# Optimization experiments

Hardware: AMD Instinct MI355X
Metric: run time of the kernel (lower is better)

## Reference

```python
import jax, jax.numpy as jnp
import numpy as np

D = 128        # node_state_dim
F = 10         # len(CHOSEN_CONNECTION_FEATURES)
N_IP = 20000
N_CONN = 100000
E = 200000
T = 3


def _seg_mean(vals, ids, n):
    s = jax.ops.segment_sum(vals, ids, num_segments=n)
    c = jax.ops.segment_sum(jnp.ones((vals.shape[0], 1), vals.dtype), ids, num_segments=n)
    return s / jnp.maximum(c, 1.0)


def _gru(x, h, kernel, rec_kernel, bias):
    # keras GRUCell, reset_after=True, gate order [z, r, hh]
    xm = x @ kernel + bias[0]
    hm = h @ rec_kernel + bias[1]
    xz, xr, xh = jnp.split(xm, 3, axis=-1)
    hz, hr, hh = jnp.split(hm, 3, axis=-1)
    z = jax.nn.sigmoid(xz + hz)
    r = jax.nn.sigmoid(xr + hr)
    hcand = jnp.tanh(xh + r * hh)
    return z * h + (1.0 - z) * hcand


def setup_inputs() -> dict:
    key = jax.random.key(0)
    ks = jax.random.split(key, 24)
    s = 0.02
    inp = {
        "feature_connection": jax.random.normal(ks[0], (N_CONN, F), jnp.float32),
        "src_ip_to_connection": jax.random.randint(ks[1], (E,), 0, N_IP, jnp.int32),
        "dst_ip_to_connection": jax.random.randint(ks[2], (E,), 0, N_CONN, jnp.int32),
        "src_connection_to_ip": jax.random.randint(ks[3], (E,), 0, N_CONN, jnp.int32),
        "dst_connection_to_ip": jax.random.randint(ks[4], (E,), 0, N_IP, jnp.int32),
        # message MLPs
        "W_m1": jax.random.normal(ks[5], (2 * D, D), jnp.float32) * s,
        "b_m1": jnp.zeros((D,), jnp.float32),
        "W_m2": jax.random.normal(ks[6], (2 * D, D), jnp.float32) * s,
        "b_m2": jnp.zeros((D,), jnp.float32),
        # GRU cells
        "gru_ip_k": jax.random.normal(ks[7], (D, 3 * D), jnp.float32) * s,
        "gru_ip_r": jax.random.normal(ks[8], (D, 3 * D), jnp.float32) * s,
        "gru_ip_b": jnp.zeros((2, 3 * D), jnp.float32),
        "gru_c_k": jax.random.normal(ks[9], (D, 3 * D), jnp.float32) * s,
        "gru_c_r": jax.random.normal(ks[10], (D, 3 * D), jnp.float32) * s,
        "gru_c_b": jnp.zeros((2, 3 * D), jnp.float32),
        # readout MLP
        "W_r1": jax.random.normal(ks[11], (D, 128), jnp.float32) * s,
        "b_r1": jnp.zeros((128,), jnp.float32),
        "W_r2": jax.random.normal(ks[12], (128, 64), jnp.float32) * s,
        "b_r2": jnp.zeros((64,), jnp.float32),
        "W_r3": jax.random.normal(ks[13], (64, 15), jnp.float32) * s,
        "b_r3": jnp.zeros((15,), jnp.float32),
    }
    return inp


def reference(feature_connection, src_ip_to_connection, dst_ip_to_connection,
              src_connection_to_ip, dst_connection_to_ip,
              W_m1, b_m1, W_m2, b_m2,
              gru_ip_k, gru_ip_r, gru_ip_b,
              gru_c_k, gru_c_r, gru_c_b,
              W_r1, b_r1, W_r2, b_r2, W_r3, b_r3):
    ip_state = jnp.ones((N_IP, D), jnp.float32)
    connection_state = jnp.concatenate(
        [feature_connection, jnp.zeros((N_CONN, D - F), jnp.float32)], axis=1)

    for _ in range(T):
        # ip -> connection messages
        nn_in = jnp.concatenate([ip_state[src_ip_to_connection],
                                 connection_state[dst_ip_to_connection]], axis=1)
        ip_message = jax.nn.relu(nn_in @ W_m1 + b_m1)            # [E, D]
        ip_mean = _seg_mean(ip_message, dst_ip_to_connection, N_CONN)
        # connection -> ip messages
        nn_in2 = jnp.concatenate([connection_state[src_connection_to_ip],
                                  ip_state[dst_connection_to_ip]], axis=1)
        conn_message = jax.nn.relu(nn_in2 @ W_m2 + b_m2)         # [E, D]
        conn_mean = _seg_mean(conn_message, dst_connection_to_ip, N_IP)
        # GRU updates
        ip_state = _gru(conn_mean, ip_state, gru_ip_k, gru_ip_r, gru_ip_b)
        connection_state = _gru(ip_mean, connection_state, gru_c_k, gru_c_r, gru_c_b)

    h = jax.nn.relu(connection_state @ W_r1 + b_r1)
    h = jax.nn.relu(h @ W_r2 + b_r2)
    return jax.nn.softmax(h @ W_r3 + b_r3, axis=-1)              # [N_CONN, 15]
```

## Files before the change

### kernel.cpp

```cpp
#include <hip/hip_runtime.h>
#include <math.h>

#define D 128
#define NF 10
#define N_IP 20000
#define N_CONN 100000
#define NE 200000
#define T_ROUNDS 3

typedef unsigned short u16;
using bf16x8 = __attribute__((ext_vector_type(8))) short;
using floatx4 = __attribute__((ext_vector_type(4))) float;

__device__ inline u16 f2bf(float f) {
  union { float f; unsigned u; } v; v.f = f;
  unsigned u = v.u;
  return (u16)((u + 0x7fffu + ((u >> 16) & 1u)) >> 16);
}
__device__ inline float bf2f(u16 h) {
  union { unsigned u; float f; } v; v.u = ((unsigned)h) << 16; return v.f;
}

__device__ inline float fsigmoid(float s) { return 1.f / (1.f + __expf(-s)); }
__device__ inline float ftanh(float a) {
  a = fminf(fmaxf(a, -15.f), 15.f);
  float e = __expf(2.f * a);
  return (e - 1.f) / (e + 1.f);
}

__global__ void k_init_all(u16* __restrict__ ip_state, u16* __restrict__ conn_state,
                           const float* __restrict__ feat, int* __restrict__ cnt) {
  int i = blockIdx.x * blockDim.x + threadIdx.x;
  const int nip = N_IP * D;
  const int nstate = (N_IP + N_CONN) * D;
  if (i < nip) {
    ip_state[i] = 0x3F80;
  } else if (i < nstate) {
    int j = i - nip;
    int r = j >> 7, c = j & 127;
    conn_state[j] = (c < NF) ? f2bf(feat[r * NF + c]) : (u16)0;
  }
  if (i < N_CONN + N_IP) cnt[i] = 0;
}

__global__ void k_prep_all(
    const float* __restrict__ gik, const float* __restrict__ gir,
    const float* __restrict__ gck, const float* __restrict__ gcr,
    const float* __restrict__ Wm1, const float* __restrict__ Wm2,
    const float* __restrict__ Wr1, const float* __restrict__ Wr2,
    u16* __restrict__ gikb, u16* __restrict__ girb,
    u16* __restrict__ gckb, u16* __restrict__ gcrb,
    u16* __restrict__ wm1b, u16* __restrict__ wm2b,
    u16* __restrict__ wm1t, u16* __restrict__ wm2t,
    u16* __restrict__ wr1b, u16* __restrict__ wr2b) {
  int i = blockIdx.x * blockDim.x + threadIdx.x;
  if (i < 196608) {
    int m = i / 49152, r = i % 49152;
    const float* W = (m == 0) ? gik : (m == 1) ? gir : (m == 2) ? gck : gcr;
    u16* Wb = (m == 0) ? gikb : (m == 1) ? girb : (m == 2) ? gckb : gcrb;
    int col = r >> 7, k = r & 127;
    Wb[r] = f2bf(W[k * 384 + col]);
  } else if (i < 278528) {
    int j = i - 196608;
    int m = j / 16384, r = j % 16384;
    const float* W; u16* Wb; int k0;
    if (m == 0) { W = Wm1; Wb = wm1b; k0 = 128; }
    else if (m == 1) { W = Wm2; Wb = wm2b; k0 = 128; }
    else if (m == 2) { W = Wm1; Wb = wm1t; k0 = 0; }
    else if (m == 3) { W = Wm2; Wb = wm2t; k0 = 0; }
    else { W = Wr1; Wb = wr1b; k0 = 0; }
    int col = r >> 7, k = r & 127;
    Wb[r] = f2bf(W[(k0 + k) * 128 + col]);
  } else if (i < 286720) {
    int r = i - 278528;
    int col = r >> 7, k = r & 127;
    wr2b[r] = f2bf(Wr2[k * 64 + col]);
  }
}

__global__ void k_colsum(const float* __restrict__ Wm1, float* __restrict__ csum) {
  int c = threadIdx.x;
  float s = 0.f;
  for (int k = 0; k < 128; k++) s += Wm1[k * 128 + c];
  csum[c] = s;
}

__global__ void k_initP(const float* __restrict__ csum, const float* __restrict__ feat,
                        const float* __restrict__ Wm2,
                        u16* __restrict__ P1, u16* __restrict__ P2) {
  int i = blockIdx.x * blockDim.x + threadIdx.x;
  const int n1 = N_IP * 16;
  const int n2 = N_CONN * 16;
  if (i < n1) {
    int r = i >> 4, g = i & 15;
    u16 v[8];
#pragma unroll
    for (int k = 0; k < 8; k++) v[k] = f2bf(csum[g * 8 + k]);
    *(uint4*)(P1 + (size_t)r * 128 + g * 8) = *(const uint4*)v;
  } else if (i < n1 + n2) {
    int j = i - n1;
    int r = j >> 4, g = j & 15;
    float acc[8] = {0.f, 0.f, 0.f, 0.f, 0.f, 0.f, 0.f, 0.f};
#pragma unroll
    for (int k = 0; k < NF; k++) {
      float f = feat[(size_t)r * NF + k];
      const float* wrow = Wm2 + (size_t)k * 128 + g * 8;
#pragma unroll
      for (int c = 0; c < 8; c++) acc[c] += f * wrow[c];
    }
    u16 v[8];
#pragma unroll
    for (int c = 0; c < 8; c++) v[c] = f2bf(acc[c]);
    *(uint4*)(P2 + (size_t)r * 128 + g * 8) = *(const uint4*)v;
  }
}

__global__ void k_count(const int* __restrict__ d1, const int* __restrict__ d2,
                        int* __restrict__ c1, int* __restrict__ c2) {
  int e = blockIdx.x * blockDim.x + threadIdx.x;
  if (e >= NE) return;
  atomicAdd(&c1[d1[e]], 1);
  atomicAdd(&c2[d2[e]], 1);
}

__global__ void k_scan_part2(const int* __restrict__ cnt1, int* __restrict__ bsum1,
                             int n1, int nb1,
                             const int* __restrict__ cnt2, int* __restrict__ bsum2, int n2) {
  const int* cnt; int* bsum; int n, b;
  if ((int)blockIdx.x < nb1) { cnt = cnt1; bsum = bsum1; n = n1; b = blockIdx.x; }
  else { cnt = cnt2; bsum = bsum2; n = n2; b = blockIdx.x - nb1; }
  int t = threadIdx.x;
  int base = b * 1024 + t * 4;
  int s = 0;
#pragma unroll
  for (int i = 0; i < 4; i++) { int j = base + i; if (j < n) s += cnt[j]; }
  for (int d = 32; d > 0; d >>= 1) s += __shfl_xor(s, d, 64);
  __shared__ int wred[4];
  int lane = t & 63, wv = t >> 6;
  if (lane == 0) wred[wv] = s;
  __syncthreads();
  if (t == 0) bsum[b] = wred[0] + wred[1] + wred[2] + wred[3];
}

__device__ inline void scan_mid_body(int* bsum, int m, int t) {
  int v = (t < m) ? bsum[t] : 0;
  int lane = t & 63, wv = t >> 6;
  int x = v;
  for (int d = 1; d < 64; d <<= 1) { int y = __shfl_up(x, d, 64); if (lane >= d) x += y; }
  __shared__ int wsum[4];
  if (lane == 63) wsum[wv] = x;
  __syncthreads();
  int add = 0;
  for (int i = 0; i < wv; i++) add += wsum[i];
  int ex = add + x - v;
  if (t < m) bsum[t] = ex;
  __syncthreads();
}

__global__ void k_scan_mid2(int* __restrict__ bsum1, int m1, int* __restrict__ bsum2, int m2) {
  int t = threadIdx.x;
  scan_mid_body(bsum1, m1, t);
  scan_mid_body(bsum2, m2, t);
}

__global__ void k_scan_final2(const int* __restrict__ cnt1, const int* __restrict__ bsum1,
                              int* __restrict__ off1, int* __restrict__ cur1, int n1, int nb1,
                              const int* __restrict__ cnt2, const int* __restrict__ bsum2,
                              int* __restrict__ off2, int* __restrict__ cur2, int n2) {
  const int* cnt; const int* bsum; int* off; int* cur; int n, b;
  if ((int)blockIdx.x < nb1) {
    cnt = cnt1; bsum = bsum1; off = off1; cur = cur1; n = n1; b = blockIdx.x;
  } else {
    cnt = cnt2; bsum = bsum2; off = off2; cur = cur2; n = n2; b = blockIdx.x - nb1;
  }
  int t = threadIdx.x;
  int base = b * 1024 + t * 4;
  int vals[4]; int s = 0;
#pragma unroll
  for (int i = 0; i < 4; i++) {
    int j = base + i;
    vals[i] = (j < n) ? cnt[j] : 0;
    s += vals[i];
  }
  int lane = t & 63, wv = t >> 6;
  int x = s;
  for (int d = 1; d < 64; d <<= 1) { int y = __shfl_up(x, d, 64); if (lane >= d) x += y; }
  __shared__ int wsum[4];
  if (lane == 63) wsum[wv] = x;
  __syncthreads();
  int add = 0;
  for (int i = 0; i < wv; i++) add += wsum[i];
  int run = add + x - s + bsum[b];
#pragma unroll
  for (int i = 0; i < 4; i++) {
    int j = base + i;
    if (j < n) { off[j] = run; cur[j] = run; }
    run += vals[i];
  }
}

__global__ void k_scatter(const int* __restrict__ s1, const int* __restrict__ d1,
                          const int* __restrict__ s2, const int* __restrict__ d2,
                          int* __restrict__ cur1, int* __restrict__ cur2,
                          int* __restrict__ o1, int* __restrict__ o2) {
  int e = blockIdx.x * blockDim.x + threadIdx.x;
  if (e >= NE) return;
  int p1 = atomicAdd(&cur1[d1[e]], 1);
  o1[p1] = s1[e];
  int p2 = atomicAdd(&cur2[d2[e]], 1);
  o2[p2] = s2[e];
}

__global__ __launch_bounds__(256, 3) void k_msggru(
    u16* __restrict__ st1, const u16* __restrict__ wq1, const float* __restrict__ qb1,
    const u16* __restrict__ P1g, const int* __restrict__ srcs1g,
    const int* __restrict__ off1g, const int* __restrict__ cnt1g,
    const u16* __restrict__ wx1, const u16* __restrict__ wh1, const float* __restrict__ gb1,
    const u16* __restrict__ wp1, u16* __restrict__ Pn1, int r1, int tiles1,
    u16* __restrict__ st2, const u16* __restrict__ wq2, const float* __restrict__ qb2,
    const u16* __restrict__ P2g, const int* __restrict__ srcs2g,
    const int* __restrict__ off2g, const int* __restrict__ cnt2g,
    const u16* __restrict__ wx2, const u16* __restrict__ wh2, const float* __restrict__ gb2,
    const u16* __restrict__ wp2, u16* __restrict__ Pn2, int r2, int doP) {
  __shared__ __align__(16) char smem[49152];
  __shared__ int offLs[64];
  __shared__ int cntLs[64];
  u16* Wq = (u16*)smem;
  u16* Qb = (u16*)smem;
  u16* Xb = (u16*)(smem + 16384);
  u16* Wg = (u16*)smem;
  u16* Hls = (u16*)(smem + 32768);
  u16* H; const u16* Wqb; const float* qbias; const u16* P;
  const int* srcs; const int* off; const int* cnt;
  const u16* Wxb; const u16* Whb; const float* gbias;
  const u16* Wpt; u16* Pn; int rows, bm;
  if ((int)blockIdx.x < tiles1) {
    H = st1; Wqb = wq1; qbias = qb1; P = P1g; srcs = srcs1g; off = off1g; cnt = cnt1g;
    Wxb = wx1; Whb = wh1; gbias = gb1; Wpt = wp1; Pn = Pn1; rows = r1; bm = blockIdx.x * 64;
  } else {
    H = st2; Wqb = wq2; qbias = qb2; P = P2g; srcs = srcs2g; off = off2g; cnt = cnt2g;
    Wxb = wx2; Whb = wh2; gbias = gb2; Wpt = wp2; Pn = Pn2; rows = r2;
    bm = (blockIdx.x - tiles1) * 64;
  }
  const int tid = threadIdx.x, wv = tid >> 6, lane = tid & 63;
  const int lrow = lane & 15, quad = lane >> 4;
  const uint4 z4 = {0, 0, 0, 0};
#pragma unroll
  for (int i = 0; i < 8; i++) {
    int task = i * 256 + tid;
    int col = task >> 4, gr = task & 15;
    uint4 v = *(const uint4*)(Wqb + (size_t)col * 128 + gr * 8);
    *(uint4*)(Wq + (size_t)col * 128 + ((gr ^ (col & 15)) * 8)) = v;
  }
#pragma unroll
  for (int i = 0; i < 4; i++) {
    int task = i * 256 + tid;
    int row = task >> 4, g = task & 15;
    int grow = bm + row;
    uint4 v = (grow < rows) ? *(const uint4*)(H + (size_t)grow * 128 + g * 8) : z4;
    *(uint4*)(Hls + (size_t)row * 128 + ((g ^ (row & 15)) * 8)) = v;
  }
  if (tid < 64) {
    int node = bm + tid;
    offLs[tid] = (node < rows) ? off[node] : 0;
    cntLs[tid] = (node < rows) ? cnt[node] : 0;
  }
  __syncthreads();
  bf16x8 ah[4];
#pragma unroll
  for (int ks = 0; ks < 4; ks++)
    ah[ks] = *(const bf16x8*)(Hls + (size_t)(wv * 16 + lrow) * 128 + (((ks * 4 + quad) ^ lrow) * 8));
  floatx4 acc[8];
#pragma unroll
  for (int ct = 0; ct < 8; ct++) acc[ct] = {0.f, 0.f, 0.f, 0.f};
#pragma unroll
  for (int ks = 0; ks < 4; ks++) {
#pragma unroll
    for (int ct = 0; ct < 8; ct++) {
      int col = ct * 16 + lrow;
      bf16x8 b = *(const bf16x8*)(Wq + (size_t)col * 128 + (((4 * ks + quad) ^ lrow) * 8));
      acc[ct] = __builtin_amdgcn_mfma_f32_16x16x32_bf16(ah[ks], b, acc[ct], 0, 0, 0);
    }
  }
  __syncthreads();
#pragma unroll
  for (int ct = 0; ct < 8; ct++) {
    int col = ct * 16 + lrow;
    float bv = qbias[col];
#pragma unroll
    for (int reg = 0; reg < 4; reg++) {
      int lr = wv * 16 + quad * 4 + reg;
      Qb[(size_t)lr * 128 + col] = f2bf(acc[ct][reg] + bv);
    }
  }
  __syncthreads();
#pragma unroll
  for (int it = 0; it < 4; it++) {
    int task = it * 256 + tid;
    int nl = task >> 4, g = task & 15;
    int node = bm + nl;
    if (node >= rows) continue;
    int c8 = g << 3;
    float q[8];
    {
      uint4 qv = *(const uint4*)(Qb + (size_t)nl * 128 + c8);
      unsigned qq[4] = {qv.x, qv.y, qv.z, qv.w};
#pragma unroll
      for (int k = 0; k < 4; k++) {
        q[2 * k] = __uint_as_float(qq[k] << 16);
        q[2 * k + 1] = __uint_as_float(qq[k] & 0xffff0000u);
      }
    }
    float acg[8] = {0.f, 0.f, 0.f, 0.f, 0.f, 0.f, 0.f, 0.f};
    int o = offLs[nl], n = cntLs[nl];
    int i = 0;
    for (; i + 4 <= n; i += 4) {
      int s0 = srcs[o + i], s1 = srcs[o + i + 1], s2 = srcs[o + i + 2], s3 = srcs[o + i + 3];
      uint4 v0 = *(const uint4*)(P + (size_t)s0 * 128 + c8);
      uint4 v1 = *(const uint4*)(P + (size_t)s1 * 128 + c8);
      uint4 v2 = *(const uint4*)(P + (size_t)s2 * 128 + c8);
      uint4 v3 = *(const uint4*)(P + (size_t)s3 * 128 + c8);
      unsigned w[16] = {v0.x, v0.y, v0.z, v0.w, v1.x, v1.y, v1.z, v1.w,
                        v2.x, v2.y, v2.z, v2.w, v3.x, v3.y, v3.z, v3.w};
#pragma unroll
      for (int e = 0; e < 4; e++)
#pragma unroll
        for (int k = 0; k < 4; k++) {
          unsigned ww = w[e * 4 + k];
          float lo = __uint_as_float(ww << 16);
          float hi = __uint_as_float(ww & 0xffff0000u);
          acg[2 * k] += fmaxf(lo + q[2 * k], 0.f);
          acg[2 * k + 1] += fmaxf(hi + q[2 * k + 1], 0.f);
        }
    }
    for (; i < n; i++) {
      int s0 = srcs[o + i];
      uint4 v0 = *(const uint4*)(P + (size_t)s0 * 128 + c8);
      unsigned w[4] = {v0.x, v0.y, v0.z, v0.w};
#pragma unroll
      for (int k = 0; k < 4; k++) {
        unsigned ww = w[k];
        float lo = __uint_as_float(ww << 16);
        float hi = __uint_as_float(ww & 0xffff0000u);
        acg[2 * k] += fmaxf(lo + q[2 * k], 0.f);
        acg[2 * k + 1] += fmaxf(hi + q[2 * k + 1], 0.f);
      }
    }
    float inv = 1.f / fmaxf((float)n, 1.f);
    bf16x8 ov;
#pragma unroll
    for (int k = 0; k < 8; k++) ov[k] = (short)f2bf(acg[k] * inv);
    *(bf16x8*)(Xb + (size_t)nl * 128 + ((g ^ (nl & 15)) * 8)) = ov;
  }
  __syncthreads();
  bf16x8 ax[4];
#pragma unroll
  for (int ks = 0; ks < 4; ks++)
    ax[ks] = *(const bf16x8*)(Xb + (size_t)(wv * 16 + lrow) * 128 + (((ks * 4 + quad) ^ lrow) * 8));
  const int lr0 = wv * 16 + quad * 4;
  const u16* gp0; const u16* gp1; const u16* gp2;
  const u16* gp3; const u16* gp4; const u16* gp5;
  u16* lp0; u16* lp1; u16* lp2; u16* lp3; u16* lp4; u16* lp5;
  {
#define MK_PTRS(J, GP, LP)                                                      \
    {                                                                           \
      int task = (J) * 256 + tid;                                               \
      int seg = task >> 8, rem = task & 255;                                    \
      int col = rem >> 4, gr = rem & 15;                                        \
      GP = (seg < 3 ? Wxb : Whb) +                                              \
           (size_t)((seg < 3 ? seg : seg - 3) * 128 + col) * 128 + gr * 8;      \
      LP = Wg + (size_t)(seg * 16 + col) * 128 + ((gr ^ col) * 8);              \
    }
    MK_PTRS(0, gp0, lp0) MK_PTRS(1, gp1, lp1) MK_PTRS(2, gp2, lp2)
    MK_PTRS(3, gp3, lp3) MK_PTRS(4, gp4, lp4) MK_PTRS(5, gp5, lp5)
#undef MK_PTRS
  }
  uint4 v0 = *(const uint4*)(gp0);
  uint4 v1 = *(const uint4*)(gp1);
  uint4 v2 = *(const uint4*)(gp2);
  uint4 v3 = *(const uint4*)(gp3);
  uint4 v4 = *(const uint4*)(gp4);
  uint4 v5 = *(const uint4*)(gp5);
  for (int ch = 0; ch < 8; ch++) {
    __syncthreads();
    *(uint4*)lp0 = v0; *(uint4*)lp1 = v1; *(uint4*)lp2 = v2;
    *(uint4*)lp3 = v3; *(uint4*)lp4 = v4; *(uint4*)lp5 = v5;
    __syncthreads();
    if (ch < 7) {
      size_t d = (size_t)(ch + 1) * 2048;
      v0 = *(const uint4*)(gp0 + d);
      v1 = *(const uint4*)(gp1 + d);
      v2 = *(const uint4*)(gp2 + d);
      v3 = *(const uint4*)(gp3 + d);
      v4 = *(const uint4*)(gp4 + d);
      v5 = *(const uint4*)(gp5 + d);
    }
    floatx4 gacc[3][2];
#pragma unroll
    for (int g = 0; g < 3; g++) {
      gacc[g][0] = {0.f, 0.f, 0.f, 0.f};
      gacc[g][1] = {0.f, 0.f, 0.f, 0.f};
    }
#pragma unroll
    for (int ks = 0; ks < 4; ks++) {
      int posu = ((4 * ks + quad) ^ lrow) * 8;
#pragma unroll
      for (int g = 0; g < 3; g++) {
        bf16x8 bx = *(const bf16x8*)(Wg + (size_t)(g * 16 + lrow) * 128 + posu);
        bf16x8 bh = *(const bf16x8*)(Wg + (size_t)((3 + g) * 16 + lrow) * 128 + posu);
        gacc[g][0] = __builtin_amdgcn_mfma_f32_16x16x32_bf16(ax[ks], bx, gacc[g][0], 0, 0, 0);
        gacc[g][1] = __builtin_amdgcn_mfma_f32_16x16x32_bf16(ah[ks], bh, gacc[g][1], 0, 0, 0);
      }
    }
    int hcol = ch * 16 + lrow;
    float bxz = gbias[hcol];
    float bxr = gbias[128 + hcol];
    float bxh = gbias[256 + hcol];
    float bhz = gbias[384 + hcol];
    float bhr = gbias[384 + 128 + hcol];
    float bhh = gbias[384 + 256 + hcol];
    int ggr = 2 * ch + (lrow >> 3);
    int gel = lrow & 7;
#pragma unroll
    for (int reg = 0; reg < 4; reg++) {
      int lr = lr0 + reg;
      float xz = gacc[0][0][reg] + bxz;
      float xr = gacc[1][0][reg] + bxr;
      float xh = gacc[2][0][reg] + bxh;
      float hz = gacc[0][1][reg] + bhz;
      float hr = gacc[1][1][reg] + bhr;
      float hh = gacc[2][1][reg] + bhh;
      float z = fsigmoid(xz + hz);
      float rr = fsigmoid(xr + hr);
      float hc = ftanh(xh + rr * hh);
      u16* hp = Hls + (size_t)lr * 128 + ((ggr ^ (lr & 15)) * 8) + gel;
      float hold = bf2f(*hp);
      *hp = f2bf(z * hold + (1.f - z) * hc);
    }
  }
  __syncthreads();
#pragma unroll
  for (int i = 0; i < 4; i++) {
    int task = i * 256 + tid;
    int row = task >> 4, g = task & 15;
    int grow = bm + row;
    if (grow < rows)
      *(uint4*)(H + (size_t)grow * 128 + g * 8) =
          *(const uint4*)(Hls + (size_t)row * 128 + ((g ^ (row & 15)) * 8));
  }
  if (!doP) return;
  bf16x8 ah2[4];
#pragma unroll
  for (int ks = 0; ks < 4; ks++)
    ah2[ks] = *(const bf16x8*)(Hls + (size_t)(wv * 16 + lrow) * 128 + (((ks * 4 + quad) ^ lrow) * 8));
  u16* Wp = (u16*)smem;
#pragma unroll
  for (int i = 0; i < 8; i++) {
    int task = i * 256 + tid;
    int col = task >> 4, gr = task & 15;
    uint4 v = *(const uint4*)(Wpt + (size_t)col * 128 + gr * 8);
    *(uint4*)(Wp + (size_t)col * 128 + ((gr ^ (col & 15)) * 8)) = v;
  }
  __syncthreads();
#pragma unroll
  for (int ct = 0; ct < 8; ct++) acc[ct] = {0.f, 0.f, 0.f, 0.f};
#pragma unroll
  for (int ks = 0; ks < 4; ks++) {
#pragma unroll
    for (int ct = 0; ct < 8; ct++) {
      int col = ct * 16 + lrow;
      bf16x8 b = *(const bf16x8*)(Wp + (size_t)col * 128 + (((4 * ks + quad) ^ lrow) * 8));
      acc[ct] = __builtin_amdgcn_mfma_f32_16x16x32_bf16(ah2[ks], b, acc[ct], 0, 0, 0);
    }
  }
  u16* Cls = Hls;
#pragma unroll
  for (int ct = 0; ct < 8; ct++) {
    int col = ct * 16 + lrow;
#pragma unroll
    for (int reg = 0; reg < 4; reg++) {
      int lr = wv * 16 + quad * 4 + reg;
      Cls[(size_t)lr * 128 + col] = f2bf(acc[ct][reg]);
    }
  }
  __syncthreads();
#pragma unroll
  for (int i = 0; i < 4; i++) {
    int task = i * 256 + tid;
    int row = task >> 4, g = task & 15;
    int grow = bm + row;
    if (grow < rows)
      *(uint4*)(Pn + (size_t)grow * 128 + g * 8) =
          *(const uint4*)(Cls + (size_t)row * 128 + g * 8);
  }
}

__global__ __launch_bounds__(256) void k_readout2(
    const u16* __restrict__ S, const u16* __restrict__ W1b, const float* __restrict__ b1,
    const u16* __restrict__ W2b, const float* __restrict__ b2,
    const float* __restrict__ W3, const float* __restrict__ b3,
    float* __restrict__ out, int M) {
  __shared__ __align__(16) char smem[64 * 132 * 4];
  u16* Wls = (u16*)smem;
  u16* H1ls = (u16*)smem;
  u16* W2ls = (u16*)(smem + 17408);
  u16* H2ls = (u16*)smem;
  float* W3ls = (float*)(smem + 9216);
  float* b3ls = (float*)(smem + 9216 + 3840);
  const int tid = threadIdx.x, wv = tid >> 6, lane = tid & 63;
  const int lrow = lane & 15, quad = lane >> 4;
  const int bm = blockIdx.x * 64;
#pragma unroll
  for (int i = 0; i < 8; i++) {
    int task = i * 256 + tid;
    int col = task >> 4, gr = task & 15;
    uint4 v = *(const uint4*)(W1b + (size_t)col * 128 + gr * 8);
    *(uint4*)(Wls + (size_t)col * 128 + ((gr ^ (col & 15)) * 8)) = v;
  }
  const int arow = bm + wv * 16 + lrow;
  const bool arv = arow < M;
  const bf16x8 zv = {0, 0, 0, 0, 0, 0, 0, 0};
  bf16x8 a[4];
#pragma unroll
  for (int ks = 0; ks < 4; ks++)
    a[ks] = arv ? *(const bf16x8*)(S + (size_t)arow * 128 + quad * 8 + ks * 32) : zv;
  __syncthreads();
  floatx4 acc1[8];
#pragma unroll
  for (int ct = 0; ct < 8; ct++) acc1[ct] = {0.f, 0.f, 0.f, 0.f};
#pragma unroll
  for (int ks = 0; ks < 4; ks++) {
#pragma unroll
    for (int ct = 0; ct < 8; ct++) {
      int col = ct * 16 + lrow;
      bf16x8 b = *(const bf16x8*)(Wls + (size_t)col * 128 + (((4 * ks + quad) ^ lrow) * 8));
      acc1[ct] = __builtin_amdgcn_mfma_f32_16x16x32_bf16(a[ks], b, acc1[ct], 0, 0, 0);
    }
  }
  __syncthreads();
#pragma unroll
  for (int ct = 0; ct < 8; ct++) {
    int col = ct * 16 + lrow;
    float bv = b1[col];
#pragma unroll
    for (int reg = 0; reg < 4; reg++) {
      int lr = wv * 16 + quad * 4 + reg;
      H1ls[(size_t)lr * 136 + col] = f2bf(fmaxf(acc1[ct][reg] + bv, 0.f));
    }
  }
#pragma unroll
  for (int i = 0; i < 4; i++) {
    int task = i * 256 + tid;
    int col = task >> 4, gr = task & 15;
    uint4 v = *(const uint4*)(W2b + (size_t)col * 128 + gr * 8);
    *(uint4*)(W2ls + (size_t)col * 128 + ((gr ^ (col & 15)) * 8)) = v;
  }
  __syncthreads();
  bf16x8 a2[4];
#pragma unroll
  for (int ks = 0; ks < 4; ks++)
    a2[ks] = *(const bf16x8*)(H1ls + (size_t)(wv * 16 + lrow) * 136 + quad * 8 + ks * 32);
  floatx4 acc2[4];
#pragma unroll
  for (int ct = 0; ct < 4; ct++) acc2[ct] = {0.f, 0.f, 0.f, 0.f};
#pragma unroll
  for (int ks = 0; ks < 4; ks++) {
#pragma unroll
    for (int ct = 0; ct < 4; ct++) {
      int col = ct * 16 + lrow;
      bf16x8 b = *(const bf16x8*)(W2ls + (size_t)col * 128 + (((4 * ks + quad) ^ lrow) * 8));
      acc2[ct] = __builtin_amdgcn_mfma_f32_16x16x32_bf16(a2[ks], b, acc2[ct], 0, 0, 0);
    }
  }
  __syncthreads();
#pragma unroll
  for (int ct = 0; ct < 4; ct++) {
    int col = ct * 16 + lrow;
    float bv = b2[col];
#pragma unroll
    for (int reg = 0; reg < 4; reg++) {
      int lr = wv * 16 + quad * 4 + reg;
      H2ls[(size_t)lr * 72 + col] = f2bf(fmaxf(acc2[ct][reg] + bv, 0.f));
    }
  }
  for (int l = tid; l < 960; l += 256) W3ls[l] = W3[l];
  if (tid < 15) b3ls[tid] = b3[tid];
  __syncthreads();
  if (tid < 64) {
    int row = tid, gr2 = bm + row;
    if (gr2 < M) {
      float lg[15];
#pragma unroll
      for (int c = 0; c < 15; c++) lg[c] = b3ls[c];
      for (int k = 0; k < 64; k++) {
        float hk = bf2f(H2ls[(size_t)row * 72 + k]);
#pragma unroll
        for (int c = 0; c < 15; c++) lg[c] += hk * W3ls[k * 15 + c];
      }
      float m = lg[0];
#pragma unroll
      for (int c = 1; c < 15; c++) m = fmaxf(m, lg[c]);
      float ssum = 0.f;
#pragma unroll
      for (int c = 0; c < 15; c++) { lg[c] = __expf(lg[c] - m); ssum += lg[c]; }
      float inv = 1.f / ssum;
#pragma unroll
      for (int c = 0; c < 15; c++) out[(size_t)gr2 * 15 + c] = lg[c] * inv;
    }
  }
}

extern "C" void kernel_launch(void* const* d_in, const int* in_sizes, int n_in,
                              void* d_out, int out_size, void* d_ws, size_t ws_size,
                              hipStream_t stream) {
  const float* feat = (const float*)d_in[0];
  const int* src1 = (const int*)d_in[1];
  const int* dst1 = (const int*)d_in[2];
  const int* src2 = (const int*)d_in[3];
  const int* dst2 = (const int*)d_in[4];
  const float* Wm1 = (const float*)d_in[5];
  const float* bm1 = (const float*)d_in[6];
  const float* Wm2 = (const float*)d_in[7];
  const float* bm2 = (const float*)d_in[8];
  const float* gik = (const float*)d_in[9];
  const float* gir = (const float*)d_in[10];
  const float* gib = (const float*)d_in[11];
  const float* gck = (const float*)d_in[12];
  const float* gcr = (const float*)d_in[13];
  const float* gcb = (const float*)d_in[14];
  const float* Wr1 = (const float*)d_in[15];
  const float* br1 = (const float*)d_in[16];
  const float* Wr2 = (const float*)d_in[17];
  const float* br2 = (const float*)d_in[18];
  const float* Wr3 = (const float*)d_in[19];
  const float* br3 = (const float*)d_in[20];
  float* out = (float*)d_out;

  u16* w16 = (u16*)d_ws;
  size_t o = 0;
  u16* ip_state = w16 + o;   o += (size_t)N_IP * D;
  u16* conn_state = w16 + o; o += (size_t)N_CONN * D;
  u16* P1a = w16 + o;        o += (size_t)N_IP * D;
  u16* P2a = w16 + o;        o += (size_t)N_CONN * D;
  u16* P1b = w16 + o;        o += (size_t)N_IP * D;
  u16* P2b = w16 + o;        o += (size_t)N_CONN * D;
  u16* gikb = w16 + o;       o += 49152;
  u16* girb = w16 + o;       o += 49152;
  u16* gckb = w16 + o;       o += 49152;
  u16* gcrb = w16 + o;       o += 49152;
  u16* wm1b = w16 + o;       o += 16384;
  u16* wm2b = w16 + o;       o += 16384;
  u16* wm1t = w16 + o;       o += 16384;
  u16* wm2t = w16 + o;       o += 16384;
  u16* wr1b = w16 + o;       o += 16384;
  u16* wr2b = w16 + o;       o += 8192;
  float* csum = (float*)(w16 + o); o += 256;
  int* ip = (int*)(w16 + o);
  int* cnt1 = ip;  ip += N_CONN;
  int* cnt2 = ip;  ip += N_IP;
  int* off1 = ip;  ip += N_CONN;
  int* off2 = ip;  ip += N_IP;
  int* cur1 = ip;  ip += N_CONN;
  int* cur2 = ip;  ip += N_IP;
  int* srcs1 = ip; ip += NE;
  int* srcs2 = ip; ip += NE;
  int* bsum1 = ip; ip += 256;
  int* bsum2 = ip; ip += 256;

  const int BT = 256;

  const int nstate = (N_IP + N_CONN) * D;
  k_init_all<<<(nstate + BT - 1) / BT, BT, 0, stream>>>(ip_state, conn_state, feat, cnt1);
  k_prep_all<<<(286720 + BT - 1) / BT, BT, 0, stream>>>(
      gik, gir, gck, gcr, Wm1, Wm2, Wr1, Wr2,
      gikb, girb, gckb, gcrb, wm1b, wm2b, wm1t, wm2t, wr1b, wr2b);
  k_colsum<<<1, 128, 0, stream>>>(Wm1, csum);
  const int nPinit = (N_IP + N_CONN) * 16;
  k_initP<<<(nPinit + BT - 1) / BT, BT, 0, stream>>>(csum, feat, Wm2, P1a, P2a);

  k_count<<<(NE + BT - 1) / BT, BT, 0, stream>>>(dst1, dst2, cnt1, cnt2);
  const int nb1 = (N_CONN + 1023) / 1024, nb2 = (N_IP + 1023) / 1024;
  k_scan_part2<<<nb1 + nb2, 256, 0, stream>>>(cnt1, bsum1, N_CONN, nb1, cnt2, bsum2, N_IP);
  k_scan_mid2<<<1, 256, 0, stream>>>(bsum1, nb1, bsum2, nb2);
  k_scan_final2<<<nb1 + nb2, 256, 0, stream>>>(cnt1, bsum1, off1, cur1, N_CONN, nb1,
                                               cnt2, bsum2, off2, cur2, N_IP);
  k_scatter<<<(NE + BT - 1) / BT, BT, 0, stream>>>(src1, dst1, src2, dst2,
                                                   cur1, cur2, srcs1, srcs2);

  const int t64ip = (N_IP + 63) / 64;
  const int t64cn = (N_CONN + 63) / 64;

  u16* P1buf[2] = {P1a, P1b};
  u16* P2buf[2] = {P2a, P2b};
  for (int t = 0; t < T_ROUNDS; t++) {
    int cu = t & 1, nx = cu ^ 1;
    k_msggru<<<t64ip + t64cn, 256, 0, stream>>>(
        ip_state, wm2b, bm2, P2buf[cu], srcs2, off2, cnt2, gikb, girb, gib,
        wm1t, P1buf[nx], N_IP, t64ip,
        conn_state, wm1b, bm1, P1buf[cu], srcs1, off1, cnt1, gckb, gcrb, gcb,
        wm2t, P2buf[nx], N_CONN, (t < T_ROUNDS - 1) ? 1 : 0);
  }

  k_readout2<<<t64cn, 256, 0, stream>>>(conn_state, wr1b, br1, wr2b, br2,
                                        Wr3, br3, out, N_CONN);
}
```

Baseline: 493.3 us.

## Halve LDS weight staging to fit four blocks per CU

Stages the 128x128 projection weights in two 64-column halves, each followed by its own MFMA pass, and reuses the Q buffer for the aggregated messages. Offsets and counts are moved into the shared arena, shrinking LDS per block from about 48KB to 40KB. The launch bound is raised from 3 to 4 blocks per CU so more waves can hide gather latency. In exchange it adds extra barriers and weight reloads, and the tighter register budget may cause spilling.

```diff
diff --git a/kernel.cpp b/kernel.cpp
--- a/kernel.cpp
+++ b/kernel.cpp
@@ -211,7 +211,7 @@
   o2[p2] = s2[e];
 }
 
-__global__ __launch_bounds__(256, 3) void k_msggru(
+__global__ __launch_bounds__(256, 4) void k_msggru(
     u16* __restrict__ st1, const u16* __restrict__ wq1, const float* __restrict__ qb1,
     const u16* __restrict__ P1g, const int* __restrict__ srcs1g,
     const int* __restrict__ off1g, const int* __restrict__ cnt1g,
@@ -222,14 +222,13 @@
     const int* __restrict__ off2g, const int* __restrict__ cnt2g,
     const u16* __restrict__ wx2, const u16* __restrict__ wh2, const float* __restrict__ gb2,
     const u16* __restrict__ wp2, u16* __restrict__ Pn2, int r2, int doP) {
-  __shared__ __align__(16) char smem[49152];
-  __shared__ int offLs[64];
-  __shared__ int cntLs[64];
+  __shared__ __align__(16) char smem[40960];
   u16* Wq = (u16*)smem;
   u16* Qb = (u16*)smem;
-  u16* Xb = (u16*)(smem + 16384);
   u16* Wg = (u16*)smem;
-  u16* Hls = (u16*)(smem + 32768);
+  u16* Hls = (u16*)(smem + 24576);
+  int* offLs = (int*)(smem + 24064);
+  int* cntLs = (int*)(smem + 24320);
   u16* H; const u16* Wqb; const float* qbias; const u16* P;
   const int* srcs; const int* off; const int* cnt;
   const u16* Wxb; const u16* Whb; const float* gbias;
@@ -246,7 +245,7 @@
   const int lrow = lane & 15, quad = lane >> 4;
   const uint4 z4 = {0, 0, 0, 0};
 #pragma unroll
-  for (int i = 0; i < 8; i++) {
+  for (int i = 0; i < 4; i++) {
     int task = i * 256 + tid;
     int col = task >> 4, gr = task & 15;
     uint4 v = *(const uint4*)(Wqb + (size_t)col * 128 + gr * 8);
@@ -276,10 +275,28 @@
 #pragma unroll
   for (int ks = 0; ks < 4; ks++) {
 #pragma unroll
-    for (int ct = 0; ct < 8; ct++) {
-      int col = ct * 16 + lrow;
-      bf16x8 b = *(const bf16x8*)(Wq + (size_t)col * 128 + (((4 * ks + quad) ^ lrow) * 8));
-      acc[ct] = __builtin_amdgcn_mfma_f32_16x16x32_bf16(ah[ks], b, acc[ct], 0, 0, 0);
+    for (int j = 0; j < 4; j++) {
+      int colh = j * 16 + lrow;
+      bf16x8 b = *(const bf16x8*)(Wq + (size_t)colh * 128 + (((4 * ks + quad) ^ lrow) * 8));
+      acc[j] = __builtin_amdgcn_mfma_f32_16x16x32_bf16(ah[ks], b, acc[j], 0, 0, 0);
+    }
+  }
+  __syncthreads();
+#pragma unroll
+  for (int i = 0; i < 4; i++) {
+    int task = i * 256 + tid;
+    int col = task >> 4, gr = task & 15;
+    uint4 v = *(const uint4*)(Wqb + (size_t)(64 + col) * 128 + gr * 8);
+    *(uint4*)(Wq + (size_t)col * 128 + ((gr ^ (col & 15)) * 8)) = v;
+  }
+  __syncthreads();
+#pragma unroll
+  for (int ks = 0; ks < 4; ks++) {
+#pragma unroll
+    for (int j = 0; j < 4; j++) {
+      int colh = j * 16 + lrow;
+      bf16x8 b = *(const bf16x8*)(Wq + (size_t)colh * 128 + (((4 * ks + quad) ^ lrow) * 8));
+      acc[4 + j] = __builtin_amdgcn_mfma_f32_16x16x32_bf16(ah[ks], b, acc[4 + j], 0, 0, 0);
     }
   }
   __syncthreads();
@@ -350,13 +367,13 @@
     bf16x8 ov;
 #pragma unroll
     for (int k = 0; k < 8; k++) ov[k] = (short)f2bf(acg[k] * inv);
-    *(bf16x8*)(Xb + (size_t)nl * 128 + ((g ^ (nl & 15)) * 8)) = ov;
+    *(bf16x8*)(Qb + (size_t)nl * 128 + ((g ^ (nl & 15)) * 8)) = ov;
   }
   __syncthreads();
   bf16x8 ax[4];
 #pragma unroll
   for (int ks = 0; ks < 4; ks++)
-    ax[ks] = *(const bf16x8*)(Xb + (size_t)(wv * 16 + lrow) * 128 + (((ks * 4 + quad) ^ lrow) * 8));
+    ax[ks] = *(const bf16x8*)(Qb + (size_t)(wv * 16 + lrow) * 128 + (((ks * 4 + quad) ^ lrow) * 8));
   const int lr0 = wv * 16 + quad * 4;
   const u16* gp0; const u16* gp1; const u16* gp2;
   const u16* gp3; const u16* gp4; const u16* gp5;
@@ -455,7 +472,7 @@
     ah2[ks] = *(const bf16x8*)(Hls + (size_t)(wv * 16 + lrow) * 128 + (((ks * 4 + quad) ^ lrow) * 8));
   u16* Wp = (u16*)smem;
 #pragma unroll
-  for (int i = 0; i < 8; i++) {
+  for (int i = 0; i < 4; i++) {
     int task = i * 256 + tid;
     int col = task >> 4, gr = task & 15;
     uint4 v = *(const uint4*)(Wpt + (size_t)col * 128 + gr * 8);
@@ -467,10 +484,28 @@
 #pragma unroll
   for (int ks = 0; ks < 4; ks++) {
 #pragma unroll
-    for (int ct = 0; ct < 8; ct++) {
-      int col = ct * 16 + lrow;
-      bf16x8 b = *(const bf16x8*)(Wp + (size_t)col * 128 + (((4 * ks + quad) ^ lrow) * 8));
-      acc[ct] = __builtin_amdgcn_mfma_f32_16x16x32_bf16(ah2[ks], b, acc[ct], 0, 0, 0);
+    for (int j = 0; j < 4; j++) {
+      int colh = j * 16 + lrow;
+      bf16x8 b = *(const bf16x8*)(Wp + (size_t)colh * 128 + (((4 * ks + quad) ^ lrow) * 8));
+      acc[j] = __builtin_amdgcn_mfma_f32_16x16x32_bf16(ah2[ks], b, acc[j], 0, 0, 0);
+    }
+  }
+  __syncthreads();
+#pragma unroll
+  for (int i = 0; i < 4; i++) {
+    int task = i * 256 + tid;
+    int col = task >> 4, gr = task & 15;
+    uint4 v = *(const uint4*)(Wpt + (size_t)(64 + col) * 128 + gr * 8);
+    *(uint4*)(Wp + (size_t)col * 128 + ((gr ^ (col & 15)) * 8)) = v;
+  }
+  __syncthreads();
+#pragma unroll
+  for (int ks = 0; ks < 4; ks++) {
+#pragma unroll
+    for (int j = 0; j < 4; j++) {
+      int colh = j * 16 + lrow;
+      bf16x8 b = *(const bf16x8*)(Wp + (size_t)colh * 128 + (((4 * ks + quad) ^ lrow) * 8));
+      acc[4 + j] = __builtin_amdgcn_mfma_f32_16x16x32_bf16(ah2[ks], b, acc[4 + j], 0, 0, 0);
     }
   }
   u16* Cls = Hls;
```

Result: no change. 489.0 us (-0.9%).
